# Kernel optimization log

Measured on AMD Instinct MI355X. Metric: run time of the kernel, lower is better.

## Reference

```python
import jax, jax.numpy as jnp
import numpy as np

N = 50000      # nodes
E = 800000     # edges (before self loops)
F_IN = 128     # input feature dim
H = 2          # attention heads
C = 64         # hidden channels per head (H*C = 128 = layer-2 input dim)
G = 64         # graphs in batch
OUT = 10       # out_channels
NEG_SLOPE = 0.2  # PyG GATConv default leaky relu slope


def setup_inputs() -> dict:
    key = jax.random.key(0)
    ks = jax.random.split(key, 16)
    sc = lambda f: np.float32(1.0 / np.sqrt(f))
    inp = {
        "x": jax.random.normal(ks[0], (N, F_IN), jnp.float32),
        "edge_index": jax.random.randint(ks[1], (2, E), 0, N, dtype=jnp.int32),
        "batch": jnp.sort(jax.random.randint(ks[2], (N,), 0, G, dtype=jnp.int32)),
        # GATConv layer 1 (lazy (-1,-1): separate src/dst projections)
        "Ws1": jax.random.normal(ks[3], (F_IN, H * C), jnp.float32) * sc(F_IN),
        "Wd1": jax.random.normal(ks[4], (F_IN, H * C), jnp.float32) * sc(F_IN),
        "as1": jax.random.normal(ks[5], (H, C), jnp.float32) * sc(C),
        "ad1": jax.random.normal(ks[6], (H, C), jnp.float32) * sc(C),
        "b1": jnp.zeros((H * C,), jnp.float32),
        # GATConv layer 2 (input dim = H*C = 128)
        "Ws2": jax.random.normal(ks[7], (H * C, H * C), jnp.float32) * sc(H * C),
        "Wd2": jax.random.normal(ks[8], (H * C, H * C), jnp.float32) * sc(H * C),
        "as2": jax.random.normal(ks[9], (H, C), jnp.float32) * sc(C),
        "ad2": jax.random.normal(ks[10], (H, C), jnp.float32) * sc(C),
        "b2": jnp.zeros((H * C,), jnp.float32),
        # final linear
        "Wl": jax.random.normal(ks[11], (H * C, OUT), jnp.float32) * sc(H * C),
        "bl": jnp.zeros((OUT,), jnp.float32),
    }
    return inp


def gat_conv(x, src, dst, Ws, Wd, att_s, att_d, b):
    # x: [N, F]; src/dst: [E'] (self loops already included)
    n = x.shape[0]
    xs = (x @ Ws).reshape(n, H, C)          # source-side projection
    xd = (x @ Wd).reshape(n, H, C)          # dest-side projection
    a_s = jnp.einsum('nhc,hc->nh', xs, att_s)   # [N, H]
    a_d = jnp.einsum('nhc,hc->nh', xd, att_d)   # [N, H]
    e = a_s[src] + a_d[dst]                      # [E', H]
    e = jnp.where(e > 0, e, NEG_SLOPE * e)       # leaky_relu
    # softmax over incoming edges per destination node (every node has a self loop)
    m = jax.ops.segment_max(e, dst, num_segments=n)
    ew = jnp.exp(e - m[dst])
    denom = jax.ops.segment_sum(ew, dst, num_segments=n)
    alpha = ew / denom[dst]                      # [E', H]
    out = jax.ops.segment_sum(alpha[:, :, None] * xs[src], dst, num_segments=n)
    return out.reshape(n, H * C) + b


def reference(x, edge_index, batch, Ws1, Wd1, as1, ad1, b1, Ws2, Wd2, as2, ad2, b2, Wl, bl):
    # add self loops once (add_self_loops=True)
    loops = jnp.arange(N, dtype=edge_index.dtype)
    src = jnp.concatenate([edge_index[0], loops])
    dst = jnp.concatenate([edge_index[1], loops])

    h = jax.nn.relu(gat_conv(x, src, dst, Ws1, Wd1, as1, ad1, b1))
    h = jax.nn.relu(gat_conv(h, src, dst, Ws2, Wd2, as2, ad2, b2))

    # global_mean_pool over batch vector
    sums = jax.ops.segment_sum(h, batch, num_segments=G)
    cnt = jax.ops.segment_sum(jnp.ones((N,), h.dtype), batch, num_segments=G)
    pooled = sums / jnp.maximum(cnt, 1.0)[:, None]

    # dropout(p=0.5) is identity in eval mode
    return pooled @ Wl + bl
```

## Files before the change

### kernel.cpp

```cpp
#include <hip/hip_runtime.h>
#include <hip/hip_bf16.h>

#define N_NODES 50000
#define N_EDGES 800000
#define EP (N_EDGES + N_NODES)
#define N_GRAPHS 64
#define F_DIM 128
#define OUT_DIM 10
#define NB 391
#define NREP 8
#define SUBCAP 384
#define EIDS_CAP 2560
#define SC_EDGES 4096
#define SC_BLOCKS ((N_EDGES + SC_EDGES - 1) / SC_EDGES)

typedef __attribute__((ext_vector_type(8))) short short8;
typedef __attribute__((ext_vector_type(4))) float f32x4;

__device__ __forceinline__ unsigned int f2bf(float f) {
    unsigned int x; __builtin_memcpy(&x, &f, 4);
    return (x + 0x7fffu + ((x >> 16) & 1u)) >> 16;
}
__device__ __forceinline__ float bf2f(unsigned int u16) {
    unsigned int x = u16 << 16;
    float f; __builtin_memcpy(&f, &x, 4); return f;
}


__global__ __launch_bounds__(256) void prep_kernel(
    const float* __restrict__ W1, const float* __restrict__ W2,
    const float* __restrict__ Wd1, const float* __restrict__ ad1,
    const float* __restrict__ Wd2, const float* __restrict__ ad2,
    unsigned short* __restrict__ Wt1, unsigned short* __restrict__ Wt2,
    float* __restrict__ weffd1, float* __restrict__ weffd2,
    uint4* __restrict__ zero_bcur , uint4* __restrict__ zero_sums ) {
    int tid = blockIdx.x * 256 + threadIdx.x;
    if (tid < 782) zero_bcur[tid] = make_uint4(0, 0, 0, 0);
    else if (tid < 782 + 2048) zero_sums[tid - 782] = make_uint4(0, 0, 0, 0);
    if (tid < 512) {
        const float* Wd = (tid < 256) ? Wd1 : Wd2;
        const float* ad = (tid < 256) ? ad1 : ad2;
        float* wout = (tid < 256) ? weffd1 : weffd2;
        int i = tid & 255, f = i >> 1, h = i & 1;
        const float4* wr = (const float4*)(Wd + f * 128 + h * 64);
        const float4* av = (const float4*)(ad + h * 64);
        float s = 0.f;
        #pragma unroll
        for (int c = 0; c < 16; ++c) {
            float4 w = wr[c], a = av[c];
            s += w.x*a.x + w.y*a.y + w.z*a.z + w.w*a.w;
        }
        wout[f * 2 + h] = s;
    }
    const float* W = (tid < 16384) ? W1 : W2;
    unsigned short* Wt = (tid < 16384) ? Wt1 : Wt2;
    int i = tid & 16383;
    int k = i >> 7, nn = i & 127;
    Wt[nn * 128 + k] = (unsigned short)f2bf(W[i]);
}


__global__ __launch_bounds__(1024) void scatter_kernel(const int* __restrict__ ei,
                                                       int* __restrict__ bcursor,
                                                       unsigned int* __restrict__ recs) {
    __shared__ unsigned int srec[SC_EDGES];
    __shared__ int hist[NB], lcur[NB], gpos[NB];
    __shared__ int excl[512];
    int t = threadIdx.x;
    int base = blockIdx.x * SC_EDGES;
    int rep = blockIdx.x & (NREP - 1);
    for (int i = t; i < NB; i += 1024) { hist[i] = 0; lcur[i] = 0; }
    __syncthreads();
    unsigned int rec_[4]; int have[4];
    #pragma unroll
    for (int j = 0; j < 4; ++j) {
        int i = base + j * 1024 + t;
        have[j] = (i < N_EDGES);
        if (have[j]) {
            int src = ei[i], dst = ei[N_EDGES + i];
            int b = dst >> 7;
            rec_[j] = ((unsigned)b << 23) | ((unsigned)(dst & 127) << 16) | (unsigned)src;
            atomicAdd(&hist[b], 1);
        }
    }
    __syncthreads();
    if (t < 512) excl[t] = (t < NB) ? hist[t] : 0;
    __syncthreads();
    for (int off = 1; off < 512; off <<= 1) {
        int v = 0;
        if (t < 512 && t >= off) v = excl[t - off];
        __syncthreads();
        if (t < 512) excl[t] += v;
        __syncthreads();
    }
    if (t < NB && hist[t] > 0) gpos[t] = atomicAdd(&bcursor[rep * NB + t], hist[t]);
    __syncthreads();
    #pragma unroll
    for (int j = 0; j < 4; ++j) {
        if (have[j]) {
            int b = rec_[j] >> 23;
            int pos = atomicAdd(&lcur[b], 1);
            srec[(excl[b] - hist[b]) + pos] = rec_[j];
        }
    }
    __syncthreads();
    int cnt = N_EDGES - base; if (cnt > SC_EDGES) cnt = SC_EDGES;
    for (int i = t; i < cnt; i += 1024) {
        unsigned int rec = srec[i];
        int b = rec >> 23;
        int gp = gpos[b] + (i - (excl[b] - hist[b]));
        if (gp < SUBCAP)
            recs[((size_t)b * NREP + rep) * SUBCAP + gp] = rec & 0x7fffffu;
    }
}

__global__ __launch_bounds__(256) void bucketize_kernel(
    const unsigned int* __restrict__ recs, const int* __restrict__ bcursor,
    unsigned short* __restrict__ eids, int2* __restrict__ rsre, int n) {
    __shared__ int ssub[NREP + 1];
    __shared__ int hist[128], excl[128], cur[128];
    __shared__ unsigned int srec[EIDS_CAP];
    int b = blockIdx.x, t = threadIdx.x;
    int nvalid = n - b * 128; if (nvalid > 128) nvalid = 128;
    if (t < 128) { hist[t] = 0; cur[t] = 0; }
    if (t == 0) {
        int run = 0; ssub[0] = 0;
        for (int r = 0; r < NREP; ++r) {
            int c = bcursor[r * NB + b]; if (c > SUBCAP) c = SUBCAP;
            run += c; ssub[r + 1] = run;
        }
    }
    __syncthreads();
    int total = ssub[NREP];
    int maxsc = EIDS_CAP - 128;
    if (total > maxsc) total = maxsc;
    const unsigned int* rb = recs + (size_t)b * NREP * SUBCAP;
    for (int i = t; i < total; i += 256) {
        int r = 0;
        while (ssub[r + 1] <= i) ++r;
        unsigned int rec = rb[r * SUBCAP + (i - ssub[r])];
        srec[i] = rec;
        atomicAdd(&hist[(rec >> 16) & 127], 1);
    }
    __syncthreads();
    if (t < nvalid) hist[t] += 1;
    __syncthreads();
    if (t < 128) excl[t] = hist[t];
    __syncthreads();
    for (int off = 1; off < 128; off <<= 1) {
        int v = 0;
        if (t < 128 && t >= off) v = excl[t - off];
        __syncthreads();
        if (t < 128) excl[t] += v;
        __syncthreads();
    }
    int base2 = b * EIDS_CAP;
    if (t < nvalid) {
        int st = excl[t] - hist[t];
        rsre[b * 128 + t] = make_int2(base2 + st, base2 + excl[t]);
        eids[base2 + st] = (unsigned short)(b * 128 + t);
        cur[t] = 1;
    }
    __syncthreads();
    for (int i = t; i < total; i += 256) {
        unsigned int rec = srec[i];
        int dl = (rec >> 16) & 127;
        int pos = atomicAdd(&cur[dl], 1);
        eids[base2 + (excl[dl] - hist[dl]) + pos] = (unsigned short)(rec & 0xffffu);
    }
}


__global__ __launch_bounds__(256) void gemm_fused_f32a_kernel(
    const float* __restrict__ A, const unsigned short* __restrict__ Wt,
    const float* __restrict__ att_s, const float* __restrict__ weffd,
    unsigned short* __restrict__ C, float* __restrict__ a_s, float* __restrict__ a_d, int n) {
    int t = threadIdx.x;
    int l = t & 63;
    int quad = l >> 4, lr = l & 15;
    int m0 = blockIdx.x * 64 + (t >> 6) * 16;
    int arow = m0 + lr; if (arow >= n) arow = n - 1;

    short8 afrag[4];
    float pd0 = 0.f, pd1 = 0.f;
    const float2* wd2 = (const float2*)weffd;
    #pragma unroll
    for (int kb = 0; kb < 4; ++kb) {
        const float4* ap = (const float4*)(A + (size_t)arow * 128 + kb * 32 + quad * 8);
        float4 a0 = ap[0], a1 = ap[1];
        int k0 = kb * 32 + quad * 8;
        float2 w0 = wd2[k0+0], w1 = wd2[k0+1], w2 = wd2[k0+2], w3 = wd2[k0+3];
        float2 w4 = wd2[k0+4], w5 = wd2[k0+5], w6 = wd2[k0+6], w7 = wd2[k0+7];
        pd0 += a0.x*w0.x + a0.y*w1.x + a0.z*w2.x + a0.w*w3.x
             + a1.x*w4.x + a1.y*w5.x + a1.z*w6.x + a1.w*w7.x;
        pd1 += a0.x*w0.y + a0.y*w1.y + a0.z*w2.y + a0.w*w3.y
             + a1.x*w4.y + a1.y*w5.y + a1.z*w6.y + a1.w*w7.y;
        short8 s;
        s[0] = (short)f2bf(a0.x); s[1] = (short)f2bf(a0.y);
        s[2] = (short)f2bf(a0.z); s[3] = (short)f2bf(a0.w);
        s[4] = (short)f2bf(a1.x); s[5] = (short)f2bf(a1.y);
        s[6] = (short)f2bf(a1.z); s[7] = (short)f2bf(a1.w);
        afrag[kb] = s;
    }
    pd0 += __shfl_xor(pd0, 16); pd0 += __shfl_xor(pd0, 32);
    pd1 += __shfl_xor(pd1, 16); pd1 += __shfl_xor(pd1, 32);
    if (l < 16 && m0 + lr < n) *(float2*)(a_d + (size_t)(m0 + lr) * 2) = make_float2(pd0, pd1);

    f32x4 acc[8] = {};
    #pragma unroll
    for (int nt = 0; nt < 8; ++nt) {
        #pragma unroll
        for (int kb = 0; kb < 4; ++kb) {
            short8 b = *(const short8*)(Wt + (size_t)(nt * 16 + lr) * 128 + kb * 32 + quad * 8);
            acc[nt] = __builtin_amdgcn_mfma_f32_16x16x32_bf16(afrag[kb], b, acc[nt], 0, 0, 0);
        }
    }
    float asv[8];
    #pragma unroll
    for (int nt = 0; nt < 8; ++nt) asv[nt] = att_s[nt * 16 + lr];
    float pa0[4] = {}, pa1[4] = {};
    #pragma unroll
    for (int nt = 0; nt < 8; ++nt)
        #pragma unroll
        for (int r = 0; r < 4; ++r) {
            if (nt < 4) pa0[r] += acc[nt][r] * asv[nt];
            else        pa1[r] += acc[nt][r] * asv[nt];
        }
    #pragma unroll
    for (int d = 1; d < 16; d <<= 1) {
        #pragma unroll
        for (int r = 0; r < 4; ++r) {
            pa0[r] += __shfl_xor(pa0[r], d);
            pa1[r] += __shfl_xor(pa1[r], d);
        }
    }
    if (lr == 0) {
        #pragma unroll
        for (int r = 0; r < 4; ++r) {
            int row = m0 + quad * 4 + r;
            if (row < n) *(float2*)(a_s + (size_t)row * 2) = make_float2(pa0[r], pa1[r]);
        }
    }
    #pragma unroll
    for (int nt = 0; nt < 8; ++nt)
        #pragma unroll
        for (int r = 0; r < 4; ++r) {
            int row = m0 + quad * 4 + r;
            if (row < n)
                C[(size_t)row * 128 + nt * 16 + lr] = (unsigned short)f2bf(acc[nt][r]);
        }
}

__global__ __launch_bounds__(256) void gemm_fused_bf16_kernel(
    const unsigned short* __restrict__ A, const unsigned short* __restrict__ Wt,
    const float* __restrict__ att_s, const float* __restrict__ weffd,
    unsigned short* __restrict__ C, float* __restrict__ a_s, float* __restrict__ a_d, int n) {
    int t = threadIdx.x;
    int l = t & 63;
    int quad = l >> 4, lr = l & 15;
    int m0 = blockIdx.x * 64 + (t >> 6) * 16;
    int arow = m0 + lr; if (arow >= n) arow = n - 1;

    short8 afrag[4];
    float pd0 = 0.f, pd1 = 0.f;
    const float2* wd2 = (const float2*)weffd;
    #pragma unroll
    for (int kb = 0; kb < 4; ++kb) {
        short8 s = *(const short8*)(A + (size_t)arow * 128 + kb * 32 + quad * 8);
        afrag[kb] = s;
        const unsigned int* u = (const unsigned int*)&s;
        int k0 = kb * 32 + quad * 8;
        #pragma unroll
        for (int d = 0; d < 4; ++d) {
            float x0 = __uint_as_float(u[d] << 16);
            float x1 = __uint_as_float(u[d] & 0xffff0000u);
            float2 wv0 = wd2[k0 + 2*d], wv1 = wd2[k0 + 2*d + 1];
            pd0 += x0 * wv0.x + x1 * wv1.x;
            pd1 += x0 * wv0.y + x1 * wv1.y;
        }
    }
    pd0 += __shfl_xor(pd0, 16); pd0 += __shfl_xor(pd0, 32);
    pd1 += __shfl_xor(pd1, 16); pd1 += __shfl_xor(pd1, 32);
    if (l < 16 && m0 + lr < n) *(float2*)(a_d + (size_t)(m0 + lr) * 2) = make_float2(pd0, pd1);

    f32x4 acc[8] = {};
    #pragma unroll
    for (int nt = 0; nt < 8; ++nt) {
        #pragma unroll
        for (int kb = 0; kb < 4; ++kb) {
            short8 b = *(const short8*)(Wt + (size_t)(nt * 16 + lr) * 128 + kb * 32 + quad * 8);
            acc[nt] = __builtin_amdgcn_mfma_f32_16x16x32_bf16(afrag[kb], b, acc[nt], 0, 0, 0);
        }
    }
    float asv[8];
    #pragma unroll
    for (int nt = 0; nt < 8; ++nt) asv[nt] = att_s[nt * 16 + lr];
    float pa0[4] = {}, pa1[4] = {};
    #pragma unroll
    for (int nt = 0; nt < 8; ++nt)
        #pragma unroll
        for (int r = 0; r < 4; ++r) {
            if (nt < 4) pa0[r] += acc[nt][r] * asv[nt];
            else        pa1[r] += acc[nt][r] * asv[nt];
        }
    #pragma unroll
    for (int d = 1; d < 16; d <<= 1) {
        #pragma unroll
        for (int r = 0; r < 4; ++r) {
            pa0[r] += __shfl_xor(pa0[r], d);
            pa1[r] += __shfl_xor(pa1[r], d);
        }
    }
    if (lr == 0) {
        #pragma unroll
        for (int r = 0; r < 4; ++r) {
            int row = m0 + quad * 4 + r;
            if (row < n) *(float2*)(a_s + (size_t)row * 2) = make_float2(pa0[r], pa1[r]);
        }
    }
    #pragma unroll
    for (int nt = 0; nt < 8; ++nt)
        #pragma unroll
        for (int r = 0; r < 4; ++r) {
            int row = m0 + quad * 4 + r;
            if (row < n)
                C[(size_t)row * 128 + nt * 16 + lr] = (unsigned short)f2bf(acc[nt][r]);
        }
}


__global__ __launch_bounds__(256) void aggregate_kernel(
    const int2* __restrict__ rsre, const unsigned short* __restrict__ eids,
    const float* __restrict__ a_s, const float* __restrict__ a_d,
    const unsigned int* __restrict__ xs32, const float* __restrict__ bias,
    unsigned int* __restrict__ out32, int n) {
    int wave = (int)((blockIdx.x * blockDim.x + threadIdx.x) >> 6);
    int lane = threadIdx.x & 63;
    if (wave >= n) return;
    int dstn = wave;
    int h    = lane >> 5;
    int j32  = lane & 31;
    int hoff = h << 5;
    int ch   = lane * 2;
    float2 advv = *(const float2*)(a_d + (size_t)dstn * 2);
    float adv = (h == 0) ? advv.x : advv.y;
    int2 rr = rsre[dstn];
    int row = rr.x, end = rr.y;

    float accA0 = 0.f, accA1 = 0.f, accB0 = 0.f, accB1 = 0.f, lsum = 0.f;
    for (int base = row; base < end; base += 32) {
        int rem = end - base;
        int k = rem < 32 ? rem : 32;
        int idx = base + (j32 < k ? j32 : k - 1);
        int eidv = (int)eids[idx];
        float2 as2 = *(const float2*)(a_s + (size_t)eidv * 2);
        float e = ((h == 0) ? as2.x : as2.y) + adv;
        e = (e > 0.f) ? e : 0.2f * e;
        float pme = (j32 < k) ? __expf(e) : 0.f;
        lsum += pme;
        int jb = 0;
        for (; jb + 4 <= k; jb += 4) {
            #pragma unroll
            for (int u = 0; u < 4; ++u) {
                int j = jb + u;
                int srcn = __shfl(eidv, j);
                float pj = __shfl(pme, j + hoff);
                unsigned int v = xs32[(size_t)srcn * 64 + lane];
                if (u & 1) {
                    accB0 += pj * __uint_as_float(v << 16);
                    accB1 += pj * __uint_as_float(v & 0xffff0000u);
                } else {
                    accA0 += pj * __uint_as_float(v << 16);
                    accA1 += pj * __uint_as_float(v & 0xffff0000u);
                }
            }
        }
        for (; jb < k; ++jb) {
            int srcn = __shfl(eidv, jb);
            float pj = __shfl(pme, jb + hoff);
            unsigned int v = xs32[(size_t)srcn * 64 + lane];
            accA0 += pj * __uint_as_float(v << 16);
            accA1 += pj * __uint_as_float(v & 0xffff0000u);
        }
    }
    #pragma unroll
    for (int d = 1; d <= 16; d <<= 1) lsum += __shfl_xor(lsum, d);
    float inv = 1.f / lsum;
    float o0 = fmaxf((accA0 + accB0) * inv + bias[ch], 0.f);
    float o1 = fmaxf((accA1 + accB1) * inv + bias[ch + 1], 0.f);
    out32[(size_t)dstn * 64 + lane] = f2bf(o0) | (f2bf(o1) << 16);
}


#define POOL_CHUNK 128

__global__ __launch_bounds__(256) void pool_partial_kernel(
    const unsigned short* __restrict__ Hf, const int* __restrict__ batch,
    float* __restrict__ sums, int n) {
    int t = threadIdx.x;
    int c = t & 127, half = t >> 7;
    int start = blockIdx.x * POOL_CHUNK;
    int end = min(start + POOL_CHUNK, n);
    float acc = 0.f;
    int cur = -1;
    for (int i = start + half; i < end; i += 2) {
        int g = batch[i];
        if (g != cur) {
            if (cur >= 0) atomicAdd(&sums[cur * 128 + c], acc);
            acc = 0.f; cur = g;
        }
        acc += bf2f(Hf[(size_t)i * 128 + c]);
    }
    if (cur >= 0) atomicAdd(&sums[cur * 128 + c], acc);
}

__global__ void final_linear_kernel(const float* __restrict__ sums,
                                    const int* __restrict__ batch,
                                    const float* __restrict__ Wl, const float* __restrict__ bl,
                                    float* __restrict__ out, int n) {
    int t = blockIdx.x * blockDim.x + threadIdx.x;
    if (t >= N_GRAPHS * OUT_DIM) return;
    int g = t / OUT_DIM, o = t % OUT_DIM;
    int lo = 0, hi = n;
    while (lo < hi) { int mid = (lo + hi) >> 1; if (batch[mid] < g) lo = mid + 1; else hi = mid; }
    int s0 = lo; hi = n;
    while (lo < hi) { int mid = (lo + hi) >> 1; if (batch[mid] < g + 1) lo = mid + 1; else hi = mid; }
    float cnt = (float)(lo - s0);
    float inv = 1.f / fmaxf(cnt, 1.f);
    float s = bl[o];
    for (int c = 0; c < 128; ++c) s += sums[g * 128 + c] * inv * Wl[c * OUT_DIM + o];
    out[g * OUT_DIM + o] = s;
}


extern "C" void kernel_launch(void* const* d_in, const int* in_sizes, int n_in,
                              void* d_out, int out_size, void* d_ws, size_t ws_size,
                              hipStream_t stream) {
    const float* x    = (const float*)d_in[0];
    const int*   ei   = (const int*)d_in[1];
    const int*   batch= (const int*)d_in[2];
    const float* Ws1  = (const float*)d_in[3];
    const float* Wd1  = (const float*)d_in[4];
    const float* as1  = (const float*)d_in[5];
    const float* ad1  = (const float*)d_in[6];
    const float* b1   = (const float*)d_in[7];
    const float* Ws2  = (const float*)d_in[8];
    const float* Wd2  = (const float*)d_in[9];
    const float* as2  = (const float*)d_in[10];
    const float* ad2  = (const float*)d_in[11];
    const float* b2   = (const float*)d_in[12];
    const float* Wl   = (const float*)d_in[13];
    const float* bl   = (const float*)d_in[14];
    float* out = (float*)d_out;

    char* p = (char*)d_ws;
    auto alloc = [&](size_t bytes) {
        void* r = (void*)p;
        p += (bytes + 255) & ~(size_t)255;
        return r;
    };
    int* bcursor  = (int*)alloc(sizeof(int) * NREP * NB);
    unsigned short* eids = (unsigned short*)alloc(sizeof(short) * (size_t)NB * EIDS_CAP);
    int2* rsre    = (int2*)alloc(sizeof(int2) * N_NODES);
    float* a_s    = (float*)alloc(sizeof(float) * N_NODES * 2);
    float* a_d    = (float*)alloc(sizeof(float) * N_NODES * 2);
    float* sums   = (float*)alloc(sizeof(float) * N_GRAPHS * 128);
    float* weffd1 = (float*)alloc(sizeof(float) * 128 * 2);
    float* weffd2 = (float*)alloc(sizeof(float) * 128 * 2);
    unsigned short* Wt1  = (unsigned short*)alloc(sizeof(short) * 128 * 128);
    unsigned short* Wt2  = (unsigned short*)alloc(sizeof(short) * 128 * 128);
    unsigned short* bufA = (unsigned short*)alloc(sizeof(short) * (size_t)N_NODES * F_DIM);
    unsigned short* bufB = (unsigned short*)alloc(sizeof(short) * (size_t)N_NODES * F_DIM);
    unsigned int* recs = (unsigned int*)bufA;

    prep_kernel<<<128, 256, 0, stream>>>(Ws1, Ws2, Wd1, ad1, Wd2, ad2,
                                         Wt1, Wt2, weffd1, weffd2,
                                         (uint4*)bcursor, (uint4*)sums);
    scatter_kernel<<<SC_BLOCKS, 1024, 0, stream>>>(ei, bcursor, recs);
    bucketize_kernel<<<NB, 256, 0, stream>>>(recs, bcursor, eids, rsre, N_NODES);

    const int gemm_grid = (N_NODES + 63) / 64;
    const int agg_grid  = (N_NODES + 3) / 4;

    gemm_fused_f32a_kernel<<<gemm_grid, 256, 0, stream>>>(x, Wt1, as1, weffd1,
                                                          bufA, a_s, a_d, N_NODES);
    aggregate_kernel<<<agg_grid, 256, 0, stream>>>(rsre, eids, a_s, a_d,
                                                   (const unsigned int*)bufA, b1,
                                                   (unsigned int*)bufB, N_NODES);

    gemm_fused_bf16_kernel<<<gemm_grid, 256, 0, stream>>>(bufB, Wt2, as2, weffd2,
                                                          bufA, a_s, a_d, N_NODES);
    aggregate_kernel<<<agg_grid, 256, 0, stream>>>(rsre, eids, a_s, a_d,
                                                   (const unsigned int*)bufA, b2,
                                                   (unsigned int*)bufB, N_NODES);

    pool_partial_kernel<<<(N_NODES + POOL_CHUNK - 1) / POOL_CHUNK, 256, 0, stream>>>(bufB, batch, sums, N_NODES);
    final_linear_kernel<<<(N_GRAPHS * OUT_DIM + 255) / 256, 256, 0, stream>>>(sums, batch, Wl, bl, out, N_NODES);
}
```

Baseline: 277.6 us.

## Process two destination nodes per wave in aggregation; fuse pooling with final linear

```diff
diff --git a/kernel.cpp b/kernel.cpp
--- a/kernel.cpp
+++ b/kernel.cpp
@@ -13,6 +13,8 @@
 #define EIDS_CAP 2560
 #define SC_EDGES 4096
 #define SC_BLOCKS ((N_EDGES + SC_EDGES - 1) / SC_EDGES)
+#define POOL_CHUNK 128
+#define POOL_BLOCKS ((N_NODES + POOL_CHUNK - 1) / POOL_CHUNK)
 
 typedef __attribute__((ext_vector_type(8))) short short8;
 typedef __attribute__((ext_vector_type(4))) float f32x4;
@@ -36,7 +38,7 @@
     uint4* __restrict__ zero_bcur , uint4* __restrict__ zero_sums ) {
     int tid = blockIdx.x * 256 + threadIdx.x;
     if (tid < 782) zero_bcur[tid] = make_uint4(0, 0, 0, 0);
-    else if (tid < 782 + 2048) zero_sums[tid - 782] = make_uint4(0, 0, 0, 0);
+    else if (tid < 782 + 2064) zero_sums[tid - 782] = make_uint4(0, 0, 0, 0);
     if (tid < 512) {
         const float* Wd = (tid < 256) ? Wd1 : Wd2;
         const float* ad = (tid < 256) ? ad1 : ad2;
@@ -329,74 +331,107 @@
 }
 
 
+#define AGG_GRP(EIV, PME, X0, X1, Y0, Y1, JB)                                   \
+    {                                                                           \
+        _Pragma("unroll")                                                       \
+        for (int u = 0; u < 4; ++u) {                                           \
+            int j = (JB) + u;                                                   \
+            int srcn = __shfl((EIV), j);                                        \
+            float pj = __shfl((PME), j + hoff);                                 \
+            unsigned int v = xs32[(size_t)srcn * 64 + lane];                    \
+            float v0 = __uint_as_float(v << 16);                                \
+            float v1 = __uint_as_float(v & 0xffff0000u);                        \
+            if (u & 1) { Y0 += pj * v0; Y1 += pj * v1; }                        \
+            else       { X0 += pj * v0; X1 += pj * v1; }                        \
+        }                                                                       \
+    }
+
 __global__ __launch_bounds__(256) void aggregate_kernel(
     const int2* __restrict__ rsre, const unsigned short* __restrict__ eids,
     const float* __restrict__ a_s, const float* __restrict__ a_d,
     const unsigned int* __restrict__ xs32, const float* __restrict__ bias,
-    unsigned int* __restrict__ out32, int n) {
-    int wave = (int)((blockIdx.x * blockDim.x + threadIdx.x) >> 6);
+    unsigned int* __restrict__ out32, int npairs) {
+    int wv = (int)((blockIdx.x * blockDim.x + threadIdx.x) >> 6);
     int lane = threadIdx.x & 63;
-    if (wave >= n) return;
-    int dstn = wave;
-    int h    = lane >> 5;
-    int j32  = lane & 31;
-    int hoff = h << 5;
-    int ch   = lane * 2;
-    float2 advv = *(const float2*)(a_d + (size_t)dstn * 2);
-    float adv = (h == 0) ? advv.x : advv.y;
-    int2 rr = rsre[dstn];
-    int row = rr.x, end = rr.y;
-
-    float accA0 = 0.f, accA1 = 0.f, accB0 = 0.f, accB1 = 0.f, lsum = 0.f;
-    for (int base = row; base < end; base += 32) {
-        int rem = end - base;
-        int k = rem < 32 ? rem : 32;
-        int idx = base + (j32 < k ? j32 : k - 1);
-        int eidv = (int)eids[idx];
-        float2 as2 = *(const float2*)(a_s + (size_t)eidv * 2);
-        float e = ((h == 0) ? as2.x : as2.y) + adv;
-        e = (e > 0.f) ? e : 0.2f * e;
-        float pme = (j32 < k) ? __expf(e) : 0.f;
-        lsum += pme;
-        int jb = 0;
-        for (; jb + 4 <= k; jb += 4) {
-            #pragma unroll
-            for (int u = 0; u < 4; ++u) {
-                int j = jb + u;
-                int srcn = __shfl(eidv, j);
-                float pj = __shfl(pme, j + hoff);
-                unsigned int v = xs32[(size_t)srcn * 64 + lane];
-                if (u & 1) {
-                    accB0 += pj * __uint_as_float(v << 16);
-                    accB1 += pj * __uint_as_float(v & 0xffff0000u);
-                } else {
-                    accA0 += pj * __uint_as_float(v << 16);
-                    accA1 += pj * __uint_as_float(v & 0xffff0000u);
-                }
-            }
-        }
-        for (; jb < k; ++jb) {
-            int srcn = __shfl(eidv, jb);
-            float pj = __shfl(pme, jb + hoff);
+    if (wv >= npairs) return;
+    int d0 = wv * 2, d1 = d0 + 1;
+    int h = lane >> 5, j32 = lane & 31, hoff = h << 5, ch = lane * 2;
+    float2 adp0 = *(const float2*)(a_d + (size_t)d0 * 2);
+    float2 adp1 = *(const float2*)(a_d + (size_t)d1 * 2);
+    float adv0 = (h == 0) ? adp0.x : adp0.y;
+    float adv1 = (h == 0) ? adp1.x : adp1.y;
+    int2 r0 = rsre[d0], r1 = rsre[d1];
+    int b0 = r0.x, e0 = r0.y, b1 = r1.x, e1 = r1.y;
+
+    float xA0 = 0, xA1 = 0, yA0 = 0, yA1 = 0;
+    float xB0 = 0, xB1 = 0, yB0 = 0, yB1 = 0;
+    float ls0 = 0, ls1 = 0;
+    while (b0 < e0 || b1 < e1) {
+        int k0 = e0 - b0; k0 = k0 < 0 ? 0 : (k0 > 32 ? 32 : k0);
+        int k1 = e1 - b1; k1 = k1 < 0 ? 0 : (k1 > 32 ? 32 : k1);
+        int ei0 = 0, ei1 = 0;
+        float pm0 = 0.f, pm1 = 0.f;
+        if (k0 > 0) {
+            ei0 = (int)eids[b0 + (j32 < k0 ? j32 : k0 - 1)];
+            float2 as2 = *(const float2*)(a_s + (size_t)ei0 * 2);
+            float ev = ((h == 0) ? as2.x : as2.y) + adv0;
+            ev = (ev > 0.f) ? ev : 0.2f * ev;
+            pm0 = (j32 < k0) ? __expf(ev) : 0.f;
+            ls0 += pm0;
+        }
+        if (k1 > 0) {
+            ei1 = (int)eids[b1 + (j32 < k1 ? j32 : k1 - 1)];
+            float2 as2 = *(const float2*)(a_s + (size_t)ei1 * 2);
+            float ev = ((h == 0) ? as2.x : as2.y) + adv1;
+            ev = (ev > 0.f) ? ev : 0.2f * ev;
+            pm1 = (j32 < k1) ? __expf(ev) : 0.f;
+            ls1 += pm1;
+        }
+        int jb0 = 0, jb1 = 0;
+        while (jb0 + 4 <= k0 && jb1 + 4 <= k1) {
+            AGG_GRP(ei0, pm0, xA0, xA1, yA0, yA1, jb0)
+            AGG_GRP(ei1, pm1, xB0, xB1, yB0, yB1, jb1)
+            jb0 += 4; jb1 += 4;
+        }
+        for (; jb0 + 4 <= k0; jb0 += 4) AGG_GRP(ei0, pm0, xA0, xA1, yA0, yA1, jb0)
+        for (; jb1 + 4 <= k1; jb1 += 4) AGG_GRP(ei1, pm1, xB0, xB1, yB0, yB1, jb1)
+        for (; jb0 < k0; ++jb0) {
+            int srcn = __shfl(ei0, jb0);
+            float pj = __shfl(pm0, jb0 + hoff);
             unsigned int v = xs32[(size_t)srcn * 64 + lane];
-            accA0 += pj * __uint_as_float(v << 16);
-            accA1 += pj * __uint_as_float(v & 0xffff0000u);
-        }
-    }
-    #pragma unroll
-    for (int d = 1; d <= 16; d <<= 1) lsum += __shfl_xor(lsum, d);
-    float inv = 1.f / lsum;
-    float o0 = fmaxf((accA0 + accB0) * inv + bias[ch], 0.f);
-    float o1 = fmaxf((accA1 + accB1) * inv + bias[ch + 1], 0.f);
-    out32[(size_t)dstn * 64 + lane] = f2bf(o0) | (f2bf(o1) << 16);
-}
-
-
-#define POOL_CHUNK 128
-
-__global__ __launch_bounds__(256) void pool_partial_kernel(
+            xA0 += pj * __uint_as_float(v << 16);
+            xA1 += pj * __uint_as_float(v & 0xffff0000u);
+        }
+        for (; jb1 < k1; ++jb1) {
+            int srcn = __shfl(ei1, jb1);
+            float pj = __shfl(pm1, jb1 + hoff);
+            unsigned int v = xs32[(size_t)srcn * 64 + lane];
+            xB0 += pj * __uint_as_float(v << 16);
+            xB1 += pj * __uint_as_float(v & 0xffff0000u);
+        }
+        b0 += k0; b1 += k1;
+    }
+    #pragma unroll
+    for (int d = 1; d <= 16; d <<= 1) {
+        ls0 += __shfl_xor(ls0, d);
+        ls1 += __shfl_xor(ls1, d);
+    }
+    float inv0 = 1.f / ls0, inv1 = 1.f / ls1;
+    float bc0 = bias[ch], bc1 = bias[ch + 1];
+    float o00 = fmaxf((xA0 + yA0) * inv0 + bc0, 0.f);
+    float o01 = fmaxf((xA1 + yA1) * inv0 + bc1, 0.f);
+    float o10 = fmaxf((xB0 + yB0) * inv1 + bc0, 0.f);
+    float o11 = fmaxf((xB1 + yB1) * inv1 + bc1, 0.f);
+    out32[(size_t)d0 * 64 + lane] = f2bf(o00) | (f2bf(o01) << 16);
+    out32[(size_t)d1 * 64 + lane] = f2bf(o10) | (f2bf(o11) << 16);
+}
+
+
+__global__ __launch_bounds__(256) void pool_final_kernel(
     const unsigned short* __restrict__ Hf, const int* __restrict__ batch,
-    float* __restrict__ sums, int n) {
+    const float* __restrict__ Wl, const float* __restrict__ bl,
+    float* __restrict__ sums, int* __restrict__ counter,
+    float* __restrict__ out, int n) {
     int t = threadIdx.x;
     int c = t & 127, half = t >> 7;
     int start = blockIdx.x * POOL_CHUNK;
@@ -412,24 +447,24 @@
         acc += bf2f(Hf[(size_t)i * 128 + c]);
     }
     if (cur >= 0) atomicAdd(&sums[cur * 128 + c], acc);
-}
-
-__global__ void final_linear_kernel(const float* __restrict__ sums,
-                                    const int* __restrict__ batch,
-                                    const float* __restrict__ Wl, const float* __restrict__ bl,
-                                    float* __restrict__ out, int n) {
-    int t = blockIdx.x * blockDim.x + threadIdx.x;
-    if (t >= N_GRAPHS * OUT_DIM) return;
-    int g = t / OUT_DIM, o = t % OUT_DIM;
-    int lo = 0, hi = n;
-    while (lo < hi) { int mid = (lo + hi) >> 1; if (batch[mid] < g) lo = mid + 1; else hi = mid; }
-    int s0 = lo; hi = n;
-    while (lo < hi) { int mid = (lo + hi) >> 1; if (batch[mid] < g + 1) lo = mid + 1; else hi = mid; }
-    float cnt = (float)(lo - s0);
-    float inv = 1.f / fmaxf(cnt, 1.f);
-    float s = bl[o];
-    for (int c = 0; c < 128; ++c) s += sums[g * 128 + c] * inv * Wl[c * OUT_DIM + o];
-    out[g * OUT_DIM + o] = s;
+    __threadfence();
+    __shared__ int lastFlag;
+    if (t == 0) lastFlag = (atomicAdd(counter, 1) == (int)gridDim.x - 1);
+    __syncthreads();
+    if (!lastFlag) return;
+    __threadfence();
+    for (int q = t; q < N_GRAPHS * OUT_DIM; q += 256) {
+        int g = q / OUT_DIM, o = q % OUT_DIM;
+        int lo = 0, hi = n;
+        while (lo < hi) { int mid = (lo + hi) >> 1; if (batch[mid] < g) lo = mid + 1; else hi = mid; }
+        int s0 = lo; hi = n;
+        while (lo < hi) { int mid = (lo + hi) >> 1; if (batch[mid] < g + 1) lo = mid + 1; else hi = mid; }
+        float cnt = (float)(lo - s0);
+        float inv = 1.f / fmaxf(cnt, 1.f);
+        float s = bl[o];
+        for (int cc = 0; cc < 128; ++cc) s += sums[g * 128 + cc] * inv * Wl[cc * OUT_DIM + o];
+        out[q] = s;
+    }
 }
 
 
@@ -464,7 +499,8 @@
     int2* rsre    = (int2*)alloc(sizeof(int2) * N_NODES);
     float* a_s    = (float*)alloc(sizeof(float) * N_NODES * 2);
     float* a_d    = (float*)alloc(sizeof(float) * N_NODES * 2);
-    float* sums   = (float*)alloc(sizeof(float) * N_GRAPHS * 128);
+    float* sums   = (float*)alloc(sizeof(float) * (N_GRAPHS * 128 + 64));
+    int* counter  = (int*)(sums + N_GRAPHS * 128);
     float* weffd1 = (float*)alloc(sizeof(float) * 128 * 2);
     float* weffd2 = (float*)alloc(sizeof(float) * 128 * 2);
     unsigned short* Wt1  = (unsigned short*)alloc(sizeof(short) * 128 * 128);
@@ -480,20 +516,21 @@
     bucketize_kernel<<<NB, 256, 0, stream>>>(recs, bcursor, eids, rsre, N_NODES);
 
     const int gemm_grid = (N_NODES + 63) / 64;
-    const int agg_grid  = (N_NODES + 3) / 4;
+    const int npairs    = N_NODES / 2;
+    const int agg_grid  = (npairs + 3) / 4;
 
     gemm_fused_f32a_kernel<<<gemm_grid, 256, 0, stream>>>(x, Wt1, as1, weffd1,
                                                           bufA, a_s, a_d, N_NODES);
     aggregate_kernel<<<agg_grid, 256, 0, stream>>>(rsre, eids, a_s, a_d,
                                                    (const unsigned int*)bufA, b1,
-                                                   (unsigned int*)bufB, N_NODES);
+                                                   (unsigned int*)bufB, npairs);
 
     gemm_fused_bf16_kernel<<<gemm_grid, 256, 0, stream>>>(bufB, Wt2, as2, weffd2,
                                                           bufA, a_s, a_d, N_NODES);
     aggregate_kernel<<<agg_grid, 256, 0, stream>>>(rsre, eids, a_s, a_d,
                                                    (const unsigned int*)bufA, b2,
-                                                   (unsigned int*)bufB, N_NODES);
-
-    pool_partial_kernel<<<(N_NODES + POOL_CHUNK - 1) / POOL_CHUNK, 256, 0, stream>>>(bufB, batch, sums, N_NODES);
-    final_linear_kernel<<<(N_GRAPHS * OUT_DIM + 255) / 256, 256, 0, stream>>>(sums, batch, Wl, bl, out, N_NODES);
-}
+                                                   (unsigned int*)bufB, npairs);
+
+    pool_final_kernel<<<POOL_BLOCKS, 256, 0, stream>>>(bufB, batch, Wl, bl,
+                                                       sums, counter, out, N_NODES);
+}
```

Measured after the change: 317.1 us. +14.2%, slower.
